# Optimization experiments

Measured on AMD Instinct MI355X. Metric: run time of the kernel, lower is better.

Reference implementation:

```python
import math
import jax, jax.numpy as jnp
import numpy as np

W_SIZE = 7
NUM_HEADS = 12


def _shift_masks(w: int, d: int):
    # upper/lower mask (applied to last row of windows)
    ul = np.zeros((w * w, w * w), np.float32)
    ul[-d * w:, :-d * w] = -np.inf
    ul[:-d * w, -d * w:] = -np.inf
    # left/right mask (applied to last column of windows)
    lr = np.zeros((w, w, w, w), np.float32)
    lr[:, -d:, :, :-d] = -np.inf
    lr[:, :-d, :, -d:] = -np.inf
    lr = lr.reshape(w * w, w * w)
    return jnp.asarray(ul), jnp.asarray(lr)


def _rel_pos_index(w: int):
    # standard Swin relative-position index, shape (w*w, w*w), values in [0, (2w-1)^2)
    coords = np.stack(np.meshgrid(np.arange(w), np.arange(w), indexing='ij'), 0).reshape(2, -1)  # (2, w*w)
    rel = coords[:, :, None] - coords[:, None, :]  # (2, ww, ww)
    idx = (rel[0] + w - 1) * (2 * w - 1) + (rel[1] + w - 1)
    return jnp.asarray(idx, dtype=jnp.int32)


def setup_inputs() -> dict:
    key = jax.random.key(0)
    ks = jax.random.split(key, 6)
    E, w = 384, W_SIZE
    return {
        'x': jax.random.normal(ks[0], (32, 56, 56, E), jnp.float32),
        'w_qkv': jax.random.normal(ks[1], (3 * E, E), jnp.float32) * 0.02,
        'b_qkv': jax.random.normal(ks[2], (3 * E,), jnp.float32) * 0.02,
        'w_proj': jax.random.normal(ks[3], (E, E), jnp.float32) * 0.02,
        'b_proj': jax.random.normal(ks[4], (E,), jnp.float32) * 0.02,
        'rel_table': jax.random.normal(ks[5], ((2 * w - 1) ** 2, NUM_HEADS), jnp.float32) * 0.02,
    }


def reference(x, w_qkv, b_qkv, w_proj, b_proj, rel_table):
    w = W_SIZE
    heads = NUM_HEADS
    B, H, Wd, C = x.shape
    hd = C // heads
    nh, nw, ww = H // w, Wd // w, w * w

    # shift (matches torch roll(shifts=(-w//2, -w//2)) == -4 for w=7)
    x = jnp.roll(x, ((-w) // 2, (-w) // 2), axis=(1, 2))

    # window partition: (B, nh, nw, ww, C)
    xw = x.reshape(B, nh, w, nw, w, C).transpose(0, 1, 3, 2, 4, 5).reshape(B, nh, nw, ww, C)

    qkv = xw @ w_qkv.T + b_qkv  # (B, nh, nw, ww, 3C)
    q, k, v = jnp.split(qkv, 3, axis=-1)

    def heads_first(t):  # (B, nh, nw, heads, ww, hd)
        return t.reshape(B, nh, nw, ww, heads, hd).transpose(0, 1, 2, 4, 3, 5)

    q, k, v = heads_first(q), heads_first(k), heads_first(v)

    attn = jnp.einsum('bhwnqd,bhwnkd->bhwnqk', q, k) * (1.0 / math.sqrt(hd))

    # relative position bias: (heads, ww, ww)
    bias = rel_table[_rel_pos_index(w)].transpose(2, 0, 1)
    attn = attn + bias

    # shift masks on last row / last column of windows
    ul, lr = _shift_masks(w, w // 2)
    mask = jnp.zeros((nh, nw, 1, ww, ww), attn.dtype)
    mask = mask.at[-1].add(ul)
    mask = mask.at[:, -1].add(lr)
    attn = attn + mask

    p = jax.nn.softmax(attn, axis=-1)
    o = jnp.einsum('bhwnqk,bhwnkd->bhwnqd', p, v)  # (B, nh, nw, heads, ww, hd)

    # merge heads and un-window
    o = o.transpose(0, 1, 2, 4, 3, 5).reshape(B, nh, nw, w, w, C)
    o = o.transpose(0, 1, 3, 2, 4, 5).reshape(B, H, Wd, C)

    o = jnp.roll(o, (w // 2, w // 2), axis=(1, 2))
    return o @ w_proj.T + b_proj
```

## Files before the change

### kernel.cpp

```cpp
#include <hip/hip_runtime.h>
#include <hip/hip_bf16.h>


typedef __bf16 bf16x8 __attribute__((ext_vector_type(8)));
typedef float  floatx4 __attribute__((ext_vector_type(4)));
typedef short  short8  __attribute__((ext_vector_type(8)));

#define MFMA16(a, b, c) __builtin_amdgcn_mfma_f32_16x16x32_bf16((a), (b), (c), 0, 0, 0)

static __device__ __forceinline__ void gload_lds16(const void* g, void* l) {
  __builtin_amdgcn_global_load_lds(
      (const __attribute__((address_space(1))) void*)g,
      (__attribute__((address_space(3))) void*)l, 16, 0, 0);
}

static __device__ __forceinline__ int src_off(int gm) {
  int win = gm / 49, t = gm - win * 49;
  int b = win >> 6, rr = win & 63;
  int wi = rr >> 3, wj = rr & 7;
  int ty = t / 7, tx = t - ty * 7;
  int y = wi * 7 + ty + 4; if (y >= 56) y -= 56;
  int x = wj * 7 + tx + 4; if (x >= 56) x -= 56;
  return ((b * 56 + y) * 56 + x) * 384;
}

static __device__ __forceinline__ int dst_off(int gm) {
  int win = gm / 49, t = gm - win * 49;
  int b = win >> 6, rr = win & 63;
  int wi = rr >> 3, wj = rr & 7;
  int ty = t / 7, tx = t - ty * 7;
  int y = wi * 7 + ty + 3; if (y >= 56) y -= 56;
  int x = wj * 7 + tx + 3; if (x >= 56) x -= 56;
  return ((b * 56 + y) * 56 + x) * 384;
}

static __device__ __forceinline__ float bf_lo(unsigned u) {
  union { unsigned v; float f; } c; c.v = u << 16; return c.f;
}
static __device__ __forceinline__ float bf_hi(unsigned u) {
  union { unsigned v; float f; } c; c.v = u & 0xFFFF0000u; return c.f;
}

__global__ __launch_bounds__(256) void prep_kernel(
    const float* __restrict__ w_qkv, const float* __restrict__ w_proj,
    const float* __restrict__ rel_table,
    __hip_bfloat16* __restrict__ wqkv_bf, __hip_bfloat16* __restrict__ wproj_bf,
    __hip_bfloat16* __restrict__ bias2) {
  const int N1 = 3 * 384 * 384;
  const int N2 = 384 * 384;
  const int N3 = 12 * 4 * 4 * 64 * 4;
  int i = blockIdx.x * 256 + threadIdx.x;
  if (i < N1) wqkv_bf[i] = __float2bfloat16(w_qkv[i]);
  int j = i - N1;
  if (j >= 0 && j < N2) wproj_bf[j] = __float2bfloat16(w_proj[j]);
  int k = i - N1 - N2;
  if (k >= 0 && k < N3) {
    int r = k & 3;
    int lp = (k >> 2) & 63;
    int ni = (k >> 8) & 3;
    int mi = (k >> 10) & 3;
    int head = k >> 12;
    int m = mi * 16 + (lp & 15);
    int n = ni * 16 + (lp >> 4) * 4 + r;
    float val = 0.f;
    if (m < 49 && n < 49) {
      int dy = m / 7 - n / 7 + 6;
      int dx = m % 7 - n % 7 + 6;
      val = rel_table[(dy * 13 + dx) * 12 + head];
    }
    bias2[k] = __float2bfloat16(val);
  }
}

__global__ __launch_bounds__(256) void xconv_kernel(
    const float* __restrict__ x, __hip_bfloat16* __restrict__ xw) {
  int gid = blockIdx.x * 256 + threadIdx.x;
  int row = gid / 48;
  int c = (gid - row * 48) * 8;
  int so = src_off(row) + c;
  floatx4 a = *(const floatx4*)(x + so);
  floatx4 b = *(const floatx4*)(x + so + 4);
  union { __hip_bfloat16 h[8]; short8 s; } u;
#pragma unroll
  for (int i = 0; i < 4; ++i) {
    u.h[i]     = __float2bfloat16(a[i]);
    u.h[4 + i] = __float2bfloat16(b[i]);
  }
  *(short8*)(xw + (size_t)row * 384 + c) = u.s;
}

__global__ __launch_bounds__(256) void qkv_kernel(
    const __hip_bfloat16* __restrict__ xw, const __hip_bfloat16* __restrict__ wq,
    const float* __restrict__ bqkv,
    __hip_bfloat16* __restrict__ qb, __hip_bfloat16* __restrict__ kb,
    __hip_bfloat16* __restrict__ vt) {
  __shared__ __hip_bfloat16 lds[2 * 16384];
  int blk = blockIdx.x;
  int b2 = (blk & 7) * 882 + (blk >> 3);
  int mt = b2 / 9, nt = b2 - mt * 9;
  int tid = threadIdx.x;
  int l = tid & 63, wv = tid >> 6;
  int wm = wv >> 1, wn = wv & 1;
  int g = l >> 4, q16 = l & 15;

  const bool swapped = (nt >= 6);
  const int aro = (swapped ? wn : wm) * 64;
  const int bro = (swapped ? wm : wn) * 64;

  int sr = tid >> 3;
  int sc = tid & 7;
  int scs = sc ^ (sr & 7);

  const __hip_bfloat16* abase = xw + (size_t)(mt * 128) * 384;
  const __hip_bfloat16* bbase = wq + (size_t)(nt * 128) * 384;

  floatx4 acc[4][4];
#pragma unroll
  for (int i = 0; i < 4; ++i)
#pragma unroll
    for (int j = 0; j < 4; ++j)
#pragma unroll
      for (int r = 0; r < 4; ++r) acc[i][j][r] = 0.f;

  auto stage = [&](int buf, int kt) {
    int k0 = kt * 64;
    __hip_bfloat16* la = lds + buf * 16384;
#pragma unroll
    for (int c = 0; c < 4; ++c) {
      int r = c * 32 + sr;
      gload_lds16(abase + (size_t)r * 384 + k0 + scs * 8, la + c * 2048 + tid * 8);
      gload_lds16(bbase + (size_t)r * 384 + k0 + scs * 8, la + 8192 + c * 2048 + tid * 8);
    }
  };

  auto compute = [&](int buf) {
    const __hip_bfloat16* la = lds + buf * 16384;
    const __hip_bfloat16* lb = la + 8192;
#pragma unroll
    for (int kk = 0; kk < 2; ++kk) {
      bf16x8 af[4], bf[4];
#pragma unroll
      for (int i = 0; i < 4; ++i) {
        int r = aro + i * 16 + q16;
        int cp = (kk * 4 + g) ^ (r & 7);
        af[i] = *(const bf16x8*)(la + r * 64 + cp * 8);
      }
#pragma unroll
      for (int i = 0; i < 4; ++i) {
        int r = bro + i * 16 + q16;
        int cp = (kk * 4 + g) ^ (r & 7);
        bf[i] = *(const bf16x8*)(lb + r * 64 + cp * 8);
      }
      if (!swapped) {
#pragma unroll
        for (int i = 0; i < 4; ++i)
#pragma unroll
          for (int j = 0; j < 4; ++j)
            acc[i][j] = MFMA16(af[i], bf[j], acc[i][j]);
      } else {
#pragma unroll
        for (int i = 0; i < 4; ++i)
#pragma unroll
          for (int j = 0; j < 4; ++j)
            acc[i][j] = MFMA16(bf[i], af[j], acc[i][j]);
      }
    }
  };

  stage(0, 0);
  stage(1, 1);
#pragma unroll
  for (int t = 0; t < 6; ++t) {
    if (t < 5) asm volatile("s_waitcnt vmcnt(8)" ::: "memory");
    else       asm volatile("s_waitcnt vmcnt(0)" ::: "memory");
    __builtin_amdgcn_s_barrier();
    __builtin_amdgcn_sched_barrier(0);
    compute(t & 1);
    if (t < 4) {
      __builtin_amdgcn_s_barrier();
      stage(t & 1, t + 2);
    }
  }

  if (!swapped) {
    const bool isq = (nt < 3);
    __hip_bfloat16* ob2 = isq ? qb : kb;
#pragma unroll
    for (int ni = 0; ni < 4; ++ni) {
      int n = nt * 128 + wn * 64 + ni * 16 + q16;
      float bn = bqkv[n];
      int nn = isq ? n : (n - 384);
#pragma unroll
      for (int mi = 0; mi < 4; ++mi) {
#pragma unroll
        for (int r = 0; r < 4; ++r) {
          int gm = mt * 128 + wm * 64 + mi * 16 + g * 4 + r;
          float v = acc[mi][ni][r] + bn;
          if (isq) v *= 0.17677669529663687f;
          ob2[gm * 384 + nn] = __float2bfloat16(v);
        }
      }
    }
  } else {
    int win4[4], t4[4];
#pragma unroll
    for (int bj = 0; bj < 4; ++bj) {
      int gm = mt * 128 + wn * 64 + bj * 16 + q16;
      int w = gm / 49;
      win4[bj] = w;
      t4[bj] = gm - w * 49;
    }
#pragma unroll
    for (int ai = 0; ai < 4; ++ai) {
#pragma unroll
      for (int r = 0; r < 4; ++r) {
        int n = nt * 128 + wm * 64 + ai * 16 + g * 4 + r;
        float bn = bqkv[n];
        int nnv = n - 768;
#pragma unroll
        for (int bj = 0; bj < 4; ++bj) {
          vt[((size_t)win4[bj] * 384 + nnv) * 64 + t4[bj]] =
              __float2bfloat16(acc[ai][bj][r] + bn);
        }
      }
    }
  }
}

__global__ __launch_bounds__(768, 4) void attnproj_kernel(
    const __hip_bfloat16* __restrict__ qb, const __hip_bfloat16* __restrict__ kb,
    const __hip_bfloat16* __restrict__ vt, const __hip_bfloat16* __restrict__ bias2,
    const __hip_bfloat16* __restrict__ wp, const float* __restrict__ bproj,
    float* __restrict__ out) {
  __shared__ __hip_bfloat16 o_lds[49][392];
  __shared__ __hip_bfloat16 p_lds[12][16][64];
  int blk = blockIdx.x;
  int win = (blk & 7) * 256 + (blk >> 3);
  int tid = threadIdx.x;
  int wv = tid >> 6, l = tid & 63;
  int g = l >> 4, q16 = l & 15;
  int wr = win & 63;
  const bool lastrow = ((wr >> 3) == 7);
  const bool lastcol = ((wr & 7) == 7);
  const int head = wv;
  const int sw = q16 & 7;

  unsigned long long badbits = 0ull;
#pragma unroll
  for (int mi = 0; mi < 4; ++mi) {
    int m = mi * 16 + q16;
    int m7 = m % 7;
    bool m28 = (m >= 28), m74 = (m7 >= 4);
#pragma unroll
    for (int ni = 0; ni < 4; ++ni) {
#pragma unroll
      for (int r = 0; r < 4; ++r) {
        int n = ni * 16 + g * 4 + r;
        bool bad = (n >= 49) ||
                   (lastrow && (m28 != (n >= 28))) ||
                   (lastcol && (m74 != ((n % 7) >= 4)));
        if (bad) badbits |= (1ull << (mi * 16 + ni * 4 + r));
      }
    }
  }

  bf16x8 zf;
#pragma unroll
  for (int i = 0; i < 8; ++i) zf[i] = (__bf16)0.0f;
  floatx4 zc;
  zc[0] = zc[1] = zc[2] = zc[3] = 0.f;

  const __hip_bfloat16* qp = qb + (size_t)(win * 49) * 384 + head * 32 + g * 8;
  const __hip_bfloat16* kp = kb + (size_t)(win * 49) * 384 + head * 32 + g * 8;

  bf16x8 aq[4], bk[4];
#pragma unroll
  for (int mi = 0; mi < 4; ++mi) {
    int row = mi * 16 + q16;
    if (row < 49) {
      aq[mi] = *(const bf16x8*)(qp + row * 384);
      bk[mi] = *(const bf16x8*)(kp + row * 384);
    } else {
      aq[mi] = zf;
      bk[mi] = zf;
    }
  }

  floatx4 st[4][4];
  __builtin_amdgcn_s_setprio(1);
#pragma unroll
  for (int ni = 0; ni < 4; ++ni)
#pragma unroll
    for (int mi = 0; mi < 4; ++mi)
      st[ni][mi] = MFMA16(bk[ni], aq[mi], zc);
  __builtin_amdgcn_s_setprio(0);

  const __hip_bfloat16* vp = vt + ((size_t)win * 384 + head * 32) * 64;
  bf16x8 bv[2][2];
#pragma unroll
  for (int ks = 0; ks < 2; ++ks)
#pragma unroll
    for (int n2 = 0; n2 < 2; ++n2)
      bv[ks][n2] = *(const bf16x8*)(vp + (n2 * 16 + q16) * 64 + ks * 32 + g * 8);

  const __hip_bfloat16* b2 = bias2 + (size_t)head * 4096;
  __hip_bfloat16* pw = &p_lds[wv][0][0];

#pragma unroll
  for (int mi = 0; mi < 4; ++mi) {
    uint2 braw[4];
#pragma unroll
    for (int ni = 0; ni < 4; ++ni)
      braw[ni] = *(const uint2*)(b2 + ((mi * 4 + ni) * 64 + l) * 4);

    float vals[4][4];
    float mx = -1e30f;
#pragma unroll
    for (int ni = 0; ni < 4; ++ni) {
#pragma unroll
      for (int r = 0; r < 4; ++r) {
        float bb = (r == 0) ? bf_lo(braw[ni].x) : (r == 1) ? bf_hi(braw[ni].x)
                   : (r == 2) ? bf_lo(braw[ni].y) : bf_hi(braw[ni].y);
        bool bad = (badbits >> (mi * 16 + ni * 4 + r)) & 1;
        float v = bad ? -1e30f : (st[ni][mi][r] + bb);
        vals[ni][r] = v;
        mx = fmaxf(mx, v);
      }
    }
    mx = fmaxf(mx, __shfl_xor(mx, 16));
    mx = fmaxf(mx, __shfl_xor(mx, 32));
    float sum = 0.f;
#pragma unroll
    for (int ni = 0; ni < 4; ++ni) {
#pragma unroll
      for (int r = 0; r < 4; ++r) {
        float p = __expf(vals[ni][r] - mx);
        vals[ni][r] = p;
        sum += p;
      }
    }
    sum += __shfl_xor(sum, 16);
    sum += __shfl_xor(sum, 32);
    float inv = 1.0f / sum;

#pragma unroll
    for (int ni = 0; ni < 4; ++ni) {
      union { __hip_bfloat16 h[4]; unsigned long long u; } pk;
#pragma unroll
      for (int r = 0; r < 4; ++r) pk.h[r] = __float2bfloat16(vals[ni][r] * inv);
      int pc = (2 * ni + (g >> 1)) ^ sw;
      *(unsigned long long*)(pw + q16 * 64 + pc * 8 + (g & 1) * 4) = pk.u;
    }

    bf16x8 av0 = *(const bf16x8*)(pw + q16 * 64 + (g ^ sw) * 8);
    bf16x8 av1 = *(const bf16x8*)(pw + q16 * 64 + ((4 + g) ^ sw) * 8);
    floatx4 o2[2];
    o2[0] = o2[1] = zc;
#pragma unroll
    for (int n2 = 0; n2 < 2; ++n2) {
      o2[n2] = MFMA16(av0, bv[0][n2], o2[n2]);
      o2[n2] = MFMA16(av1, bv[1][n2], o2[n2]);
    }
#pragma unroll
    for (int r = 0; r < 4; ++r) {
      int m = mi * 16 + g * 4 + r;
      if (m < 49) {
#pragma unroll
        for (int n2 = 0; n2 < 2; ++n2)
          o_lds[m][head * 32 + n2 * 16 + q16] = __float2bfloat16(o2[n2][r]);
      }
    }
  }

  __syncthreads();

  floatx4 pacc[4][2];
#pragma unroll
  for (int i = 0; i < 4; ++i)
#pragma unroll
    for (int j = 0; j < 2; ++j)
#pragma unroll
      for (int r = 0; r < 4; ++r) pacc[i][j][r] = 0.f;

  for (int k0 = 0; k0 < 384; k0 += 32) {
    bf16x8 af[4], bfr[2];
#pragma unroll
    for (int mi = 0; mi < 4; ++mi) {
      int row = mi * 16 + q16;
      row = row < 49 ? row : 48;
      af[mi] = *(const bf16x8*)&o_lds[row][k0 + g * 8];
    }
#pragma unroll
    for (int ni = 0; ni < 2; ++ni) {
      int brow = wv * 32 + ni * 16 + q16;
      bfr[ni] = *(const bf16x8*)(wp + (size_t)brow * 384 + k0 + g * 8);
    }
    __builtin_amdgcn_s_setprio(1);
#pragma unroll
    for (int mi = 0; mi < 4; ++mi)
#pragma unroll
      for (int ni = 0; ni < 2; ++ni)
        pacc[mi][ni] = MFMA16(af[mi], bfr[ni], pacc[mi][ni]);
    __builtin_amdgcn_s_setprio(0);
  }

#pragma unroll
  for (int mi = 0; mi < 4; ++mi) {
#pragma unroll
    for (int r = 0; r < 4; ++r) {
      int m = mi * 16 + g * 4 + r;
      if (m < 49) {
        int off = dst_off(win * 49 + m);
#pragma unroll
        for (int ni = 0; ni < 2; ++ni) {
          int n = wv * 32 + ni * 16 + q16;
          out[off + n] = pacc[mi][ni][r] + bproj[n];
        }
      }
    }
  }
}

extern "C" void kernel_launch(void* const* d_in, const int* in_sizes, int n_in,
                              void* d_out, int out_size, void* d_ws, size_t ws_size,
                              hipStream_t stream) {
  const float* x         = (const float*)d_in[0];
  const float* w_qkv     = (const float*)d_in[1];
  const float* b_qkv     = (const float*)d_in[2];
  const float* w_proj    = (const float*)d_in[3];
  const float* b_proj    = (const float*)d_in[4];
  const float* rel_table = (const float*)d_in[5];
  float* out = (float*)d_out;

  char* ws = (char*)d_ws;
  const size_t OFF_WQKV  = 0;
  const size_t OFF_WPROJ = 884736;
  const size_t OFF_BIAS2 = 1179648;
  const size_t OFF_Q     = 1572864;
  const size_t OFF_K     = OFF_Q + 77070336;
  const size_t OFF_VT    = OFF_K + 77070336;

  __hip_bfloat16* wqkv_bf  = (__hip_bfloat16*)(ws + OFF_WQKV);
  __hip_bfloat16* wproj_bf = (__hip_bfloat16*)(ws + OFF_WPROJ);
  __hip_bfloat16* bias2    = (__hip_bfloat16*)(ws + OFF_BIAS2);
  __hip_bfloat16* qb       = (__hip_bfloat16*)(ws + OFF_Q);
  __hip_bfloat16* kb       = (__hip_bfloat16*)(ws + OFF_K);
  __hip_bfloat16* vt       = (__hip_bfloat16*)(ws + OFF_VT);
  __hip_bfloat16* xw       = (__hip_bfloat16*)d_out;


  prep_kernel<<<3072, 256, 0, stream>>>(w_qkv, w_proj, rel_table, wqkv_bf, wproj_bf, bias2);
  xconv_kernel<<<18816, 256, 0, stream>>>(x, xw);
  qkv_kernel<<<7056, 256, 0, stream>>>(xw, wqkv_bf, b_qkv, qb, kb, vt);
  attnproj_kernel<<<2048, 768, 0, stream>>>(qb, kb, vt, bias2, wproj_bf, b_proj, out);
}
```

Baseline: 404.3 us.

## Fuse conversion, QKV GEMM, attention and projection into one per-window kernel

Replaces the separate x-conversion, QKV GEMM and attention+projection kernels with a single per-window kernel. It gathers the shifted window into LDS, computes Q and K directly into LDS, and writes only V^T to global memory (read back by the same block). This removes the large Q/K global round trips and two launches. Padding columns are now masked by setting the bias to -1e30. The cost is that the QKV GEMM is no longer tiled across windows: weights are reloaded from global per window with no LDS staging, and the larger LDS footprint lowers occupancy. V^T is written and reread through global memory within the block, with __syncthreads as the only ordering.

```diff
diff --git a/kernel.cpp b/kernel.cpp
--- a/kernel.cpp
+++ b/kernel.cpp
@@ -7,12 +7,6 @@
 typedef short  short8  __attribute__((ext_vector_type(8)));
 
 #define MFMA16(a, b, c) __builtin_amdgcn_mfma_f32_16x16x32_bf16((a), (b), (c), 0, 0, 0)
-
-static __device__ __forceinline__ void gload_lds16(const void* g, void* l) {
-  __builtin_amdgcn_global_load_lds(
-      (const __attribute__((address_space(1))) void*)g,
-      (__attribute__((address_space(3))) void*)l, 16, 0, 0);
-}
 
 static __device__ __forceinline__ int src_off(int gm) {
   int win = gm / 49, t = gm - win * 49;
@@ -62,7 +56,7 @@
     int head = k >> 12;
     int m = mi * 16 + (lp & 15);
     int n = ni * 16 + (lp >> 4) * 4 + r;
-    float val = 0.f;
+    float val = -1e30f;
     if (m < 49 && n < 49) {
       int dy = m / 7 - n / 7 + 6;
       int dx = m % 7 - n % 7 + 6;
@@ -72,349 +66,286 @@
   }
 }
 
-__global__ __launch_bounds__(256) void xconv_kernel(
-    const float* __restrict__ x, __hip_bfloat16* __restrict__ xw) {
-  int gid = blockIdx.x * 256 + threadIdx.x;
-  int row = gid / 48;
-  int c = (gid - row * 48) * 8;
-  int so = src_off(row) + c;
-  floatx4 a = *(const floatx4*)(x + so);
-  floatx4 b = *(const floatx4*)(x + so + 4);
-  union { __hip_bfloat16 h[8]; short8 s; } u;
-#pragma unroll
-  for (int i = 0; i < 4; ++i) {
-    u.h[i]     = __float2bfloat16(a[i]);
-    u.h[4 + i] = __float2bfloat16(b[i]);
-  }
-  *(short8*)(xw + (size_t)row * 384 + c) = u.s;
-}
-
-__global__ __launch_bounds__(256) void qkv_kernel(
-    const __hip_bfloat16* __restrict__ xw, const __hip_bfloat16* __restrict__ wq,
-    const float* __restrict__ bqkv,
-    __hip_bfloat16* __restrict__ qb, __hip_bfloat16* __restrict__ kb,
-    __hip_bfloat16* __restrict__ vt) {
-  __shared__ __hip_bfloat16 lds[2 * 16384];
-  int blk = blockIdx.x;
-  int b2 = (blk & 7) * 882 + (blk >> 3);
-  int mt = b2 / 9, nt = b2 - mt * 9;
-  int tid = threadIdx.x;
-  int l = tid & 63, wv = tid >> 6;
-  int wm = wv >> 1, wn = wv & 1;
-  int g = l >> 4, q16 = l & 15;
-
-  const bool swapped = (nt >= 6);
-  const int aro = (swapped ? wn : wm) * 64;
-  const int bro = (swapped ? wm : wn) * 64;
-
-  int sr = tid >> 3;
-  int sc = tid & 7;
-  int scs = sc ^ (sr & 7);
-
-  const __hip_bfloat16* abase = xw + (size_t)(mt * 128) * 384;
-  const __hip_bfloat16* bbase = wq + (size_t)(nt * 128) * 384;
-
-  floatx4 acc[4][4];
-#pragma unroll
-  for (int i = 0; i < 4; ++i)
-#pragma unroll
-    for (int j = 0; j < 4; ++j)
-#pragma unroll
-      for (int r = 0; r < 4; ++r) acc[i][j][r] = 0.f;
-
-  auto stage = [&](int buf, int kt) {
-    int k0 = kt * 64;
-    __hip_bfloat16* la = lds + buf * 16384;
-#pragma unroll
-    for (int c = 0; c < 4; ++c) {
-      int r = c * 32 + sr;
-      gload_lds16(abase + (size_t)r * 384 + k0 + scs * 8, la + c * 2048 + tid * 8);
-      gload_lds16(bbase + (size_t)r * 384 + k0 + scs * 8, la + 8192 + c * 2048 + tid * 8);
-    }
-  };
-
-  auto compute = [&](int buf) {
-    const __hip_bfloat16* la = lds + buf * 16384;
-    const __hip_bfloat16* lb = la + 8192;
-#pragma unroll
-    for (int kk = 0; kk < 2; ++kk) {
-      bf16x8 af[4], bf[4];
-#pragma unroll
-      for (int i = 0; i < 4; ++i) {
-        int r = aro + i * 16 + q16;
-        int cp = (kk * 4 + g) ^ (r & 7);
-        af[i] = *(const bf16x8*)(la + r * 64 + cp * 8);
-      }
-#pragma unroll
-      for (int i = 0; i < 4; ++i) {
-        int r = bro + i * 16 + q16;
-        int cp = (kk * 4 + g) ^ (r & 7);
-        bf[i] = *(const bf16x8*)(lb + r * 64 + cp * 8);
-      }
-      if (!swapped) {
-#pragma unroll
-        for (int i = 0; i < 4; ++i)
-#pragma unroll
-          for (int j = 0; j < 4; ++j)
-            acc[i][j] = MFMA16(af[i], bf[j], acc[i][j]);
-      } else {
-#pragma unroll
-        for (int i = 0; i < 4; ++i)
-#pragma unroll
-          for (int j = 0; j < 4; ++j)
-            acc[i][j] = MFMA16(bf[i], af[j], acc[i][j]);
-      }
-    }
-  };
-
-  stage(0, 0);
-  stage(1, 1);
-#pragma unroll
-  for (int t = 0; t < 6; ++t) {
-    if (t < 5) asm volatile("s_waitcnt vmcnt(8)" ::: "memory");
-    else       asm volatile("s_waitcnt vmcnt(0)" ::: "memory");
-    __builtin_amdgcn_s_barrier();
-    __builtin_amdgcn_sched_barrier(0);
-    compute(t & 1);
-    if (t < 4) {
-      __builtin_amdgcn_s_barrier();
-      stage(t & 1, t + 2);
-    }
-  }
-
-  if (!swapped) {
-    const bool isq = (nt < 3);
-    __hip_bfloat16* ob2 = isq ? qb : kb;
-#pragma unroll
-    for (int ni = 0; ni < 4; ++ni) {
-      int n = nt * 128 + wn * 64 + ni * 16 + q16;
-      float bn = bqkv[n];
-      int nn = isq ? n : (n - 384);
-#pragma unroll
-      for (int mi = 0; mi < 4; ++mi) {
-#pragma unroll
-        for (int r = 0; r < 4; ++r) {
-          int gm = mt * 128 + wm * 64 + mi * 16 + g * 4 + r;
-          float v = acc[mi][ni][r] + bn;
-          if (isq) v *= 0.17677669529663687f;
-          ob2[gm * 384 + nn] = __float2bfloat16(v);
-        }
-      }
-    }
-  } else {
-    int win4[4], t4[4];
-#pragma unroll
-    for (int bj = 0; bj < 4; ++bj) {
-      int gm = mt * 128 + wn * 64 + bj * 16 + q16;
-      int w = gm / 49;
-      win4[bj] = w;
-      t4[bj] = gm - w * 49;
-    }
-#pragma unroll
-    for (int ai = 0; ai < 4; ++ai) {
-#pragma unroll
-      for (int r = 0; r < 4; ++r) {
-        int n = nt * 128 + wm * 64 + ai * 16 + g * 4 + r;
-        float bn = bqkv[n];
-        int nnv = n - 768;
-#pragma unroll
-        for (int bj = 0; bj < 4; ++bj) {
-          vt[((size_t)win4[bj] * 384 + nnv) * 64 + t4[bj]] =
-              __float2bfloat16(acc[ai][bj][r] + bn);
-        }
-      }
-    }
-  }
-}
-
-__global__ __launch_bounds__(768, 4) void attnproj_kernel(
-    const __hip_bfloat16* __restrict__ qb, const __hip_bfloat16* __restrict__ kb,
-    const __hip_bfloat16* __restrict__ vt, const __hip_bfloat16* __restrict__ bias2,
+__global__ __launch_bounds__(768, 3) void mega_kernel(
+    const float* __restrict__ x, const __hip_bfloat16* __restrict__ wq,
+    const float* __restrict__ bqkv, const __hip_bfloat16* __restrict__ bias2,
     const __hip_bfloat16* __restrict__ wp, const float* __restrict__ bproj,
-    float* __restrict__ out) {
-  __shared__ __hip_bfloat16 o_lds[49][392];
+    __hip_bfloat16* __restrict__ vt, float* __restrict__ out) {
+  __shared__ __hip_bfloat16 xo_lds[49][392];
+  __shared__ __hip_bfloat16 q_lds[49][392];
+  __shared__ __hip_bfloat16 k_lds[49][392];
   __shared__ __hip_bfloat16 p_lds[12][16][64];
+
   int blk = blockIdx.x;
   int win = (blk & 7) * 256 + (blk >> 3);
   int tid = threadIdx.x;
   int wv = tid >> 6, l = tid & 63;
   int g = l >> 4, q16 = l & 15;
-  int wr = win & 63;
-  const bool lastrow = ((wr >> 3) == 7);
-  const bool lastcol = ((wr & 7) == 7);
-  const int head = wv;
   const int sw = q16 & 7;
 
-  unsigned long long badbits = 0ull;
-#pragma unroll
-  for (int mi = 0; mi < 4; ++mi) {
-    int m = mi * 16 + q16;
-    int m7 = m % 7;
-    bool m28 = (m >= 28), m74 = (m7 >= 4);
-#pragma unroll
-    for (int ni = 0; ni < 4; ++ni) {
-#pragma unroll
-      for (int r = 0; r < 4; ++r) {
-        int n = ni * 16 + g * 4 + r;
-        bool bad = (n >= 49) ||
-                   (lastrow && (m28 != (n >= 28))) ||
-                   (lastcol && (m74 != ((n % 7) >= 4)));
-        if (bad) badbits |= (1ull << (mi * 16 + ni * 4 + r));
-      }
-    }
-  }
-
-  bf16x8 zf;
-#pragma unroll
-  for (int i = 0; i < 8; ++i) zf[i] = (__bf16)0.0f;
   floatx4 zc;
   zc[0] = zc[1] = zc[2] = zc[3] = 0.f;
 
-  const __hip_bfloat16* qp = qb + (size_t)(win * 49) * 384 + head * 32 + g * 8;
-  const __hip_bfloat16* kp = kb + (size_t)(win * 49) * 384 + head * 32 + g * 8;
-
-  bf16x8 aq[4], bk[4];
-#pragma unroll
-  for (int mi = 0; mi < 4; ++mi) {
-    int row = mi * 16 + q16;
-    if (row < 49) {
-      aq[mi] = *(const bf16x8*)(qp + row * 384);
-      bk[mi] = *(const bf16x8*)(kp + row * 384);
-    } else {
-      aq[mi] = zf;
-      bk[mi] = zf;
-    }
-  }
-
-  floatx4 st[4][4];
-  __builtin_amdgcn_s_setprio(1);
-#pragma unroll
-  for (int ni = 0; ni < 4; ++ni)
-#pragma unroll
-    for (int mi = 0; mi < 4; ++mi)
-      st[ni][mi] = MFMA16(bk[ni], aq[mi], zc);
-  __builtin_amdgcn_s_setprio(0);
-
-  const __hip_bfloat16* vp = vt + ((size_t)win * 384 + head * 32) * 64;
-  bf16x8 bv[2][2];
-#pragma unroll
-  for (int ks = 0; ks < 2; ++ks)
-#pragma unroll
-    for (int n2 = 0; n2 < 2; ++n2)
-      bv[ks][n2] = *(const bf16x8*)(vp + (n2 * 16 + q16) * 64 + ks * 32 + g * 8);
-
-  const __hip_bfloat16* b2 = bias2 + (size_t)head * 4096;
-  __hip_bfloat16* pw = &p_lds[wv][0][0];
-
-#pragma unroll
-  for (int mi = 0; mi < 4; ++mi) {
-    uint2 braw[4];
-#pragma unroll
-    for (int ni = 0; ni < 4; ++ni)
-      braw[ni] = *(const uint2*)(b2 + ((mi * 4 + ni) * 64 + l) * 4);
-
-    float vals[4][4];
-    float mx = -1e30f;
-#pragma unroll
-    for (int ni = 0; ni < 4; ++ni) {
-#pragma unroll
-      for (int r = 0; r < 4; ++r) {
-        float bb = (r == 0) ? bf_lo(braw[ni].x) : (r == 1) ? bf_hi(braw[ni].x)
-                   : (r == 2) ? bf_lo(braw[ni].y) : bf_hi(braw[ni].y);
-        bool bad = (badbits >> (mi * 16 + ni * 4 + r)) & 1;
-        float v = bad ? -1e30f : (st[ni][mi][r] + bb);
-        vals[ni][r] = v;
-        mx = fmaxf(mx, v);
-      }
-    }
-    mx = fmaxf(mx, __shfl_xor(mx, 16));
-    mx = fmaxf(mx, __shfl_xor(mx, 32));
-    float sum = 0.f;
-#pragma unroll
-    for (int ni = 0; ni < 4; ++ni) {
-#pragma unroll
-      for (int r = 0; r < 4; ++r) {
-        float p = __expf(vals[ni][r] - mx);
-        vals[ni][r] = p;
-        sum += p;
-      }
-    }
-    sum += __shfl_xor(sum, 16);
-    sum += __shfl_xor(sum, 32);
-    float inv = 1.0f / sum;
-
-#pragma unroll
-    for (int ni = 0; ni < 4; ++ni) {
-      union { __hip_bfloat16 h[4]; unsigned long long u; } pk;
-#pragma unroll
-      for (int r = 0; r < 4; ++r) pk.h[r] = __float2bfloat16(vals[ni][r] * inv);
-      int pc = (2 * ni + (g >> 1)) ^ sw;
-      *(unsigned long long*)(pw + q16 * 64 + pc * 8 + (g & 1) * 4) = pk.u;
-    }
-
-    bf16x8 av0 = *(const bf16x8*)(pw + q16 * 64 + (g ^ sw) * 8);
-    bf16x8 av1 = *(const bf16x8*)(pw + q16 * 64 + ((4 + g) ^ sw) * 8);
-    floatx4 o2[2];
-    o2[0] = o2[1] = zc;
-#pragma unroll
-    for (int n2 = 0; n2 < 2; ++n2) {
-      o2[n2] = MFMA16(av0, bv[0][n2], o2[n2]);
-      o2[n2] = MFMA16(av1, bv[1][n2], o2[n2]);
-    }
-#pragma unroll
-    for (int r = 0; r < 4; ++r) {
-      int m = mi * 16 + g * 4 + r;
-      if (m < 49) {
-#pragma unroll
-        for (int n2 = 0; n2 < 2; ++n2)
-          o_lds[m][head * 32 + n2 * 16 + q16] = __float2bfloat16(o2[n2][r]);
-      }
-    }
-  }
-
+  for (int i = tid; i < 49 * 48; i += 768) {
+    int row = i / 48, c8 = (i - row * 48) * 8;
+    int so = src_off(win * 49 + row) + c8;
+    floatx4 a = *(const floatx4*)(x + so);
+    floatx4 b = *(const floatx4*)(x + so + 4);
+    union { __hip_bfloat16 h[8]; short8 s; } u;
+#pragma unroll
+    for (int e = 0; e < 4; ++e) {
+      u.h[e]     = __float2bfloat16(a[e]);
+      u.h[4 + e] = __float2bfloat16(b[e]);
+    }
+    *(short8*)&xo_lds[row][c8] = u.s;
+  }
   __syncthreads();
 
-  floatx4 pacc[4][2];
-#pragma unroll
-  for (int i = 0; i < 4; ++i)
-#pragma unroll
-    for (int j = 0; j < 2; ++j)
-#pragma unroll
-      for (int r = 0; r < 4; ++r) pacc[i][j][r] = 0.f;
-
-  for (int k0 = 0; k0 < 384; k0 += 32) {
-    bf16x8 af[4], bfr[2];
+  {
+    const bool isv = (wv >= 8);
+    const bool isq = (wv < 4);
+    __hip_bfloat16* dst = isq ? &q_lds[0][0] : &k_lds[0][0];
+#pragma unroll 1
+    for (int pass = 0; pass < 2; ++pass) {
+      int n0 = wv * 96 + pass * 48;
+      floatx4 acc[12];
+#pragma unroll
+      for (int i = 0; i < 12; ++i) acc[i] = zc;
+
+#pragma unroll
+      for (int ks = 0; ks < 12; ++ks) {
+        int k0 = ks * 32;
+        bf16x8 af[4], bf[3];
+#pragma unroll
+        for (int mi = 0; mi < 4; ++mi) {
+          int row = mi * 16 + q16;
+          row = row < 49 ? row : 48;
+          af[mi] = *(const bf16x8*)&xo_lds[row][k0 + g * 8];
+        }
+#pragma unroll
+        for (int ni = 0; ni < 3; ++ni)
+          bf[ni] = *(const bf16x8*)(wq + (size_t)(n0 + ni * 16 + q16) * 384 + k0 + g * 8);
+        __builtin_amdgcn_s_setprio(1);
+        if (!isv) {
+#pragma unroll
+          for (int mi = 0; mi < 4; ++mi)
+#pragma unroll
+            for (int ni = 0; ni < 3; ++ni)
+              acc[mi * 3 + ni] = MFMA16(af[mi], bf[ni], acc[mi * 3 + ni]);
+        } else {
+#pragma unroll
+          for (int ai = 0; ai < 3; ++ai)
+#pragma unroll
+            for (int bj = 0; bj < 4; ++bj)
+              acc[ai * 4 + bj] = MFMA16(bf[ai], af[bj], acc[ai * 4 + bj]);
+        }
+        __builtin_amdgcn_s_setprio(0);
+      }
+
+      if (!isv) {
+#pragma unroll
+        for (int ni = 0; ni < 3; ++ni) {
+          int n = n0 + ni * 16 + q16;
+          float bn = bqkv[n];
+          int nn = isq ? n : (n - 384);
+#pragma unroll
+          for (int mi = 0; mi < 4; ++mi) {
+#pragma unroll
+            for (int r = 0; r < 4; ++r) {
+              int m = mi * 16 + g * 4 + r;
+              if (m < 49) {
+                float v = acc[mi * 3 + ni][r] + bn;
+                if (isq) v *= 0.17677669529663687f;
+                dst[m * 392 + nn] = __float2bfloat16(v);
+              }
+            }
+          }
+        }
+      } else {
+#pragma unroll
+        for (int ai = 0; ai < 3; ++ai) {
+#pragma unroll
+          for (int r = 0; r < 4; ++r) {
+            int n = n0 + ai * 16 + g * 4 + r;
+            float bn = bqkv[n];
+            int d = n - 768;
+#pragma unroll
+            for (int bj = 0; bj < 4; ++bj) {
+              int t = bj * 16 + q16;
+              vt[((size_t)win * 384 + d) * 64 + t] =
+                  __float2bfloat16(acc[ai * 4 + bj][r] + bn);
+            }
+          }
+        }
+      }
+    }
+  }
+  __syncthreads();
+
+  {
+    const int head = wv;
+    int wr = win & 63;
+    const bool lastrow = ((wr >> 3) == 7);
+    const bool lastcol = ((wr & 7) == 7);
+
+    unsigned long long badbits = 0ull;
+    if (lastrow || lastcol) {
+#pragma unroll
+      for (int mi = 0; mi < 4; ++mi) {
+        int m = mi * 16 + q16;
+        int m7 = m % 7;
+        bool m28 = (m >= 28), m74 = (m7 >= 4);
+#pragma unroll
+        for (int ni = 0; ni < 4; ++ni) {
+#pragma unroll
+          for (int r = 0; r < 4; ++r) {
+            int n = ni * 16 + g * 4 + r;
+            bool bad = (lastrow && (m28 != (n >= 28))) ||
+                       (lastcol && (m74 != ((n % 7) >= 4)));
+            if (bad) badbits |= (1ull << (mi * 16 + ni * 4 + r));
+          }
+        }
+      }
+    }
+
+    bf16x8 aq[4], bk[4];
 #pragma unroll
     for (int mi = 0; mi < 4; ++mi) {
       int row = mi * 16 + q16;
       row = row < 49 ? row : 48;
-      af[mi] = *(const bf16x8*)&o_lds[row][k0 + g * 8];
-    }
-#pragma unroll
-    for (int ni = 0; ni < 2; ++ni) {
-      int brow = wv * 32 + ni * 16 + q16;
-      bfr[ni] = *(const bf16x8*)(wp + (size_t)brow * 384 + k0 + g * 8);
-    }
+      aq[mi] = *(const bf16x8*)&q_lds[row][head * 32 + g * 8];
+      bk[mi] = *(const bf16x8*)&k_lds[row][head * 32 + g * 8];
+    }
+
+    floatx4 st[4][4];
     __builtin_amdgcn_s_setprio(1);
 #pragma unroll
-    for (int mi = 0; mi < 4; ++mi)
-#pragma unroll
-      for (int ni = 0; ni < 2; ++ni)
-        pacc[mi][ni] = MFMA16(af[mi], bfr[ni], pacc[mi][ni]);
+    for (int ni = 0; ni < 4; ++ni)
+#pragma unroll
+      for (int mi = 0; mi < 4; ++mi)
+        st[ni][mi] = MFMA16(bk[ni], aq[mi], zc);
     __builtin_amdgcn_s_setprio(0);
-  }
-
-#pragma unroll
-  for (int mi = 0; mi < 4; ++mi) {
-#pragma unroll
-    for (int r = 0; r < 4; ++r) {
-      int m = mi * 16 + g * 4 + r;
-      if (m < 49) {
-        int off = dst_off(win * 49 + m);
-#pragma unroll
-        for (int ni = 0; ni < 2; ++ni) {
-          int n = wv * 32 + ni * 16 + q16;
-          out[off + n] = pacc[mi][ni][r] + bproj[n];
+
+    const __hip_bfloat16* vp = vt + ((size_t)win * 384 + head * 32) * 64;
+    bf16x8 bv[2][2];
+#pragma unroll
+    for (int ks = 0; ks < 2; ++ks)
+#pragma unroll
+      for (int n2 = 0; n2 < 2; ++n2)
+        bv[ks][n2] = *(const bf16x8*)(vp + (n2 * 16 + q16) * 64 + ks * 32 + g * 8);
+
+    const __hip_bfloat16* b2 = bias2 + (size_t)head * 4096;
+    __hip_bfloat16* pw = &p_lds[wv][0][0];
+
+#pragma unroll
+    for (int mi = 0; mi < 4; ++mi) {
+      uint2 braw[4];
+#pragma unroll
+      for (int ni = 0; ni < 4; ++ni)
+        braw[ni] = *(const uint2*)(b2 + ((mi * 4 + ni) * 64 + l) * 4);
+
+      float vals[4][4];
+      float mx = -1e30f;
+#pragma unroll
+      for (int ni = 0; ni < 4; ++ni) {
+#pragma unroll
+        for (int r = 0; r < 4; ++r) {
+          float bb = (r == 0) ? bf_lo(braw[ni].x) : (r == 1) ? bf_hi(braw[ni].x)
+                     : (r == 2) ? bf_lo(braw[ni].y) : bf_hi(braw[ni].y);
+          float v = st[ni][mi][r] + bb;
+          if ((badbits >> (mi * 16 + ni * 4 + r)) & 1) v = -1e30f;
+          vals[ni][r] = v;
+          mx = fmaxf(mx, v);
+        }
+      }
+      mx = fmaxf(mx, __shfl_xor(mx, 16));
+      mx = fmaxf(mx, __shfl_xor(mx, 32));
+      float sum = 0.f;
+#pragma unroll
+      for (int ni = 0; ni < 4; ++ni) {
+#pragma unroll
+        for (int r = 0; r < 4; ++r) {
+          float p = __expf(vals[ni][r] - mx);
+          vals[ni][r] = p;
+          sum += p;
+        }
+      }
+      sum += __shfl_xor(sum, 16);
+      sum += __shfl_xor(sum, 32);
+      float inv = 1.0f / sum;
+
+#pragma unroll
+      for (int ni = 0; ni < 4; ++ni) {
+        union { __hip_bfloat16 h[4]; unsigned long long u; } pk;
+#pragma unroll
+        for (int r = 0; r < 4; ++r) pk.h[r] = __float2bfloat16(vals[ni][r] * inv);
+        int pc = (2 * ni + (g >> 1)) ^ sw;
+        *(unsigned long long*)(pw + q16 * 64 + pc * 8 + (g & 1) * 4) = pk.u;
+      }
+
+      bf16x8 av0 = *(const bf16x8*)(pw + q16 * 64 + (g ^ sw) * 8);
+      bf16x8 av1 = *(const bf16x8*)(pw + q16 * 64 + ((4 + g) ^ sw) * 8);
+      floatx4 o2[2];
+      o2[0] = o2[1] = zc;
+#pragma unroll
+      for (int n2 = 0; n2 < 2; ++n2) {
+        o2[n2] = MFMA16(av0, bv[0][n2], o2[n2]);
+        o2[n2] = MFMA16(av1, bv[1][n2], o2[n2]);
+      }
+#pragma unroll
+      for (int r = 0; r < 4; ++r) {
+        int m = mi * 16 + g * 4 + r;
+        if (m < 49) {
+#pragma unroll
+          for (int n2 = 0; n2 < 2; ++n2)
+            xo_lds[m][head * 32 + n2 * 16 + q16] = __float2bfloat16(o2[n2][r]);
+        }
+      }
+    }
+  }
+  __syncthreads();
+
+  {
+    floatx4 pacc[4][2];
+#pragma unroll
+    for (int i = 0; i < 4; ++i)
+#pragma unroll
+      for (int j = 0; j < 2; ++j) pacc[i][j] = zc;
+
+    for (int k0 = 0; k0 < 384; k0 += 32) {
+      bf16x8 af[4], bfr[2];
+#pragma unroll
+      for (int mi = 0; mi < 4; ++mi) {
+        int row = mi * 16 + q16;
+        row = row < 49 ? row : 48;
+        af[mi] = *(const bf16x8*)&xo_lds[row][k0 + g * 8];
+      }
+#pragma unroll
+      for (int ni = 0; ni < 2; ++ni) {
+        int brow = wv * 32 + ni * 16 + q16;
+        bfr[ni] = *(const bf16x8*)(wp + (size_t)brow * 384 + k0 + g * 8);
+      }
+      __builtin_amdgcn_s_setprio(1);
+#pragma unroll
+      for (int mi = 0; mi < 4; ++mi)
+#pragma unroll
+        for (int ni = 0; ni < 2; ++ni)
+          pacc[mi][ni] = MFMA16(af[mi], bfr[ni], pacc[mi][ni]);
+      __builtin_amdgcn_s_setprio(0);
+    }
+
+#pragma unroll
+    for (int mi = 0; mi < 4; ++mi) {
+#pragma unroll
+      for (int r = 0; r < 4; ++r) {
+        int m = mi * 16 + g * 4 + r;
+        if (m < 49) {
+          int off = dst_off(win * 49 + m);
+#pragma unroll
+          for (int ni = 0; ni < 2; ++ni) {
+            int n = wv * 32 + ni * 16 + q16;
+            out[off + n] = pacc[mi][ni][r] + bproj[n];
+          }
         }
       }
     }
@@ -436,21 +367,14 @@
   const size_t OFF_WQKV  = 0;
   const size_t OFF_WPROJ = 884736;
   const size_t OFF_BIAS2 = 1179648;
-  const size_t OFF_Q     = 1572864;
-  const size_t OFF_K     = OFF_Q + 77070336;
-  const size_t OFF_VT    = OFF_K + 77070336;
+  const size_t OFF_VT    = 1572864;
 
   __hip_bfloat16* wqkv_bf  = (__hip_bfloat16*)(ws + OFF_WQKV);
   __hip_bfloat16* wproj_bf = (__hip_bfloat16*)(ws + OFF_WPROJ);
   __hip_bfloat16* bias2    = (__hip_bfloat16*)(ws + OFF_BIAS2);
-  __hip_bfloat16* qb       = (__hip_bfloat16*)(ws + OFF_Q);
-  __hip_bfloat16* kb       = (__hip_bfloat16*)(ws + OFF_K);
   __hip_bfloat16* vt       = (__hip_bfloat16*)(ws + OFF_VT);
-  __hip_bfloat16* xw       = (__hip_bfloat16*)d_out;
 
 
   prep_kernel<<<3072, 256, 0, stream>>>(w_qkv, w_proj, rel_table, wqkv_bf, wproj_bf, bias2);
-  xconv_kernel<<<18816, 256, 0, stream>>>(x, xw);
-  qkv_kernel<<<7056, 256, 0, stream>>>(xw, wqkv_bf, b_qkv, qb, kb, vt);
-  attnproj_kernel<<<2048, 768, 0, stream>>>(qb, kb, vt, bias2, wproj_bf, b_proj, out);
-}
+  mega_kernel<<<2048, 768, 0, stream>>>(x, wqkv_bf, b_qkv, bias2, wproj_bf, b_proj, vt, out);
+}
```

After: 400.9 us. Within noise of the previous version (-0.8%).
